# Kernel tuning notes

Hardware: AMD Instinct MI355X
Metric: run time of the kernel (lower is better)

Reference implementation:

```python
import jax, jax.numpy as jnp
import numpy as np

D = 512  # d_model
B, H, W = 32, 32, 32


def _conv1x1(x, w, b):
    # x: [B,C,H,W], w: [O,C], b: [O] -> [B,O,H,W]
    return jnp.einsum('oc,bchw->bohw', w, x) + b[None, :, None, None]


def setup_inputs() -> dict:
    key = jax.random.key(0)
    ks = jax.random.split(key, 16)
    std = 0.01  # init.normal_(m.weight, 0, 0.01)
    inp = {
        'out0': jax.random.normal(ks[0], (B, D, H, W), jnp.float32),
        'out1': jax.random.normal(ks[1], (B, D, H, W), jnp.float32),
        'out2': jax.random.normal(ks[2], (B, D, H, W), jnp.float32),
        'gamma': jax.random.uniform(ks[3], (1,), jnp.float32),
        'gamma_1': jax.random.uniform(ks[4], (1,), jnp.float32),
        'gamma_2': jax.random.uniform(ks[5], (1,), jnp.float32),
        'W_in1': std * jax.random.normal(ks[6], (D, D), jnp.float32),
        'b_in1': jnp.zeros((D,), jnp.float32),
        'W_in2': std * jax.random.normal(ks[7], (D, D), jnp.float32),
        'b_in2': jnp.zeros((D,), jnp.float32),
        'W_in3': std * jax.random.normal(ks[8], (D, D), jnp.float32),
        'b_in3': jnp.zeros((D,), jnp.float32),
        'W_trans': std * jax.random.normal(ks[9], (3 * D, 3 * D), jnp.float32),
        'b_trans': jnp.zeros((3 * D,), jnp.float32),
        'W_out1': std * jax.random.normal(ks[10], (D, D), jnp.float32),
        'b_out1': jnp.zeros((D,), jnp.float32),
        'W_out2': std * jax.random.normal(ks[11], (D, D), jnp.float32),
        'b_out2': jnp.zeros((D,), jnp.float32),
        'W_out3': std * jax.random.normal(ks[12], (D, D), jnp.float32),
        'b_out3': jnp.zeros((D,), jnp.float32),
    }
    return inp


def reference(out0, out1, out2, gamma, gamma_1, gamma_2,
              W_in1, b_in1, W_in2, b_in2, W_in3, b_in3,
              W_trans, b_trans, W_out1, b_out1, W_out2, b_out2,
              W_out3, b_out3):
    out_sim = gamma[0] * out0
    out_sim_1 = gamma_1[0] * out1
    out_sim_2 = gamma_2[0] * out2
    H_1 = _conv1x1(out_sim, W_in1, b_in1)
    H_2 = _conv1x1(out_sim_1, W_in2, b_in2)
    H_3 = _conv1x1(out_sim_2, W_in3, b_in3)
    H_cat = jnp.concatenate((H_1, H_2, H_3), axis=1)  # [B,3D,H,W]
    H_tra = _conv1x1(H_cat, W_trans, b_trans)
    s0, s1, s2 = H_tra[:, :D], H_tra[:, D:2 * D], H_tra[:, 2 * D:]
    H_4 = jax.nn.sigmoid(_conv1x1(s0, W_out1, b_out1))
    H_5 = jax.nn.sigmoid(_conv1x1(s1, W_out2, b_out2))
    H_6 = jax.nn.sigmoid(_conv1x1(s2, W_out3, b_out3))
    H_st = jnp.stack((H_4, H_5, H_6), axis=0)  # [3,B,D,H,W]
    H_all = jax.nn.softmax(H_st, axis=0)
    fused = H_all[0] * out_sim + H_all[1] * out_sim_1 + H_all[2] * out_sim_2
    return fused
```

## Files before the change

### kernel.cpp

```cpp
#include <hip/hip_runtime.h>
#include <hip/hip_bf16.h>

#define NPIX 32768
#define DCH 512
#define HWSZ 1024
#define WSQ (DCH * DCH)
#define WTR (3 * DCH * 3 * DCH)

typedef __bf16 bf16x8_t __attribute__((ext_vector_type(8)));
typedef float f32x4_t __attribute__((ext_vector_type(4)));
typedef float f32x16_t __attribute__((ext_vector_type(16)));
typedef int i32x4_t __attribute__((ext_vector_type(4)));
typedef int i32x8_t __attribute__((ext_vector_type(8)));
typedef unsigned short u16x8_t __attribute__((ext_vector_type(8)));
typedef unsigned short u16x4_t __attribute__((ext_vector_type(4)));

static __device__ __forceinline__ unsigned short f2bf(float f) {
    return __builtin_bit_cast(unsigned short, __float2bfloat16(f));
}
static __device__ __forceinline__ float bf2f(unsigned short u) {
    unsigned v = (unsigned)u << 16;
    return __builtin_bit_cast(float, v);
}

__global__ __launch_bounds__(256)
void cvt_all(const float* __restrict__ w0, const float* __restrict__ w1,
             const float* __restrict__ w2, const float* __restrict__ w3,
             const float* __restrict__ w4, const float* __restrict__ w5,
             const float* __restrict__ w6,
             __hip_bfloat16* __restrict__ d, unsigned char* __restrict__ d8,
             const float* __restrict__ b0, const float* __restrict__ b1,
             const float* __restrict__ b2, const float* __restrict__ b3,
             const float* __restrict__ b4, const float* __restrict__ b5,
             float* __restrict__ biasd)
{
    const int NB = (6 * WSQ + WTR) >> 10;
    const int bid = blockIdx.x;
    if (bid == 2 * NB) {
        for (int idx = threadIdx.x; idx < 3072; idx += 256) {
            const int r = idx >> 9, off = idx & 511;
            const float* s = (r == 0) ? b0 : (r == 1) ? b1 : (r == 2) ? b2
                           : (r == 3) ? b3 : (r == 4) ? b4 : b5;
            biasd[idx] = s[off];
        }
        return;
    }
    const bool do8 = (bid >= NB);
    const int i = ((do8 ? bid - NB : bid) * 256 + threadIdx.x) * 4;
    const float* src;
    int off;
    if (i < 3 * WSQ) {
        int r = i >> 18;
        src = (r == 0) ? w0 : ((r == 1) ? w1 : w2);
        off = i - r * WSQ;
    } else if (i < 3 * WSQ + WTR) {
        src = w3; off = i - 3 * WSQ;
    } else {
        int j = i - 3 * WSQ - WTR;
        int r = j >> 18;
        src = (r == 0) ? w4 : ((r == 1) ? w5 : w6);
        off = j - r * WSQ;
    }
    float4 f = *(const float4*)(src + off);
    if (do8) {
        int dw = __builtin_amdgcn_cvt_pk_fp8_f32(f.x, f.y, 0, false);
        dw     = __builtin_amdgcn_cvt_pk_fp8_f32(f.z, f.w, dw, true);
        *(int*)(d8 + i) = dw;
    } else {
        u16x4_t v;
        v[0] = f2bf(f.x); v[1] = f2bf(f.y); v[2] = f2bf(f.z); v[3] = f2bf(f.w);
        *(u16x4_t*)((unsigned short*)d + i) = v;
    }
}

__global__ __launch_bounds__(256)
void stage_transpose(const float* __restrict__ x0, const float* __restrict__ x1,
                     const float* __restrict__ x2,
                     const float* __restrict__ gp0, const float* __restrict__ gp1,
                     const float* __restrict__ gp2,
                     __hip_bfloat16* __restrict__ XbT,
                     unsigned char* __restrict__ Xb8, int emit8)
{
    __shared__ float tile[64][65];
    const int hw0 = blockIdx.x * 64;
    const int c0  = blockIdx.y * 64;
    const int bz  = blockIdx.z;
    const int br  = bz >> 5;
    const int b   = bz & 31;
    const float* x = (br == 0) ? x0 : ((br == 1) ? x1 : x2);
    const float g  = ((br == 0) ? gp0 : ((br == 1) ? gp1 : gp2))[0];
    const int t = threadIdx.x;

    const int qh = (t & 15) * 4;
    const int rb = t >> 4;
    const float* src = x + (size_t)b * (DCH * HWSZ) + (size_t)c0 * HWSZ + hw0;
#pragma unroll
    for (int i = 0; i < 4; ++i) {
        const int ci = rb + i * 16;
        float4 v = *(const float4*)(src + (size_t)ci * HWSZ + qh);
        v.x *= g; v.y *= g; v.z *= g; v.w *= g;
        *(float4*)&tile[ci][qh] = v;
    }
    __syncthreads();

    const int hwr = t >> 2;
    const int cch = (t & 3) * 16;
    const size_t nrow = (size_t)br * NPIX + b * HWSZ + hw0 + hwr;
    float vals[16];
#pragma unroll
    for (int e = 0; e < 16; ++e) vals[e] = tile[cch + e][hwr];

    __hip_bfloat16* dst = XbT + nrow * DCH + c0 + cch;
    u16x8_t v0, v1;
#pragma unroll
    for (int e = 0; e < 8; ++e) v0[e] = f2bf(vals[e]);
#pragma unroll
    for (int e = 0; e < 8; ++e) v1[e] = f2bf(vals[8 + e]);
    *(u16x8_t*)dst = v0;
    *((u16x8_t*)dst + 1) = v1;

    if (emit8) {
        i32x4_t w;
#pragma unroll
        for (int q = 0; q < 4; ++q) {
            int dw = __builtin_amdgcn_cvt_pk_fp8_f32(vals[4 * q], vals[4 * q + 1], 0, false);
            dw     = __builtin_amdgcn_cvt_pk_fp8_f32(vals[4 * q + 2], vals[4 * q + 3], dw, true);
            w[q] = dw;
        }
        *(i32x4_t*)(Xb8 + nrow * DCH + c0 + cch) = w;
    }
}

struct pair4 { i32x4_t lo, hi; };

__global__ __launch_bounds__(256, 2)
void gemm_f8(const unsigned char* __restrict__ A, int lda,
             const unsigned char* __restrict__ B, int ldb,
             const float* __restrict__ bias,
             void* __restrict__ Cv, int ldc, int coff0,
             int K, int NO, int TPB, int brA, int brB,
             int bstride, int cstride, int cmode)
{
    __shared__ __align__(16) unsigned char smem[73728];
    const int tid  = threadIdx.x;
    const int lane = tid & 63;
    const int wave = tid >> 6;
    const int wm = wave >> 1, wn = wave & 1;
    const int l31 = lane & 31;
    const int h   = lane >> 5;

    const int per  = gridDim.x >> 3;
    const int flat = (blockIdx.x & 7) * per + (blockIdx.x >> 3);
    const int br   = flat / TPB;
    const int rem  = flat - br * TPB;
    const int nt = rem / NO, ot = rem % NO;
    const int n0 = nt * 256, o0 = ot * 128;
    const int NT = K >> 6;

    A    += (size_t)br * (size_t)brA;
    B    += (size_t)br * (size_t)brB;
    bias += br * bstride;
    const int coff = coff0 + br * cstride;

    auto stage = [&](int t, unsigned bufb) {
#pragma unroll
        for (int p = 0; p < 6; ++p) {
            const int f = tid + p * 256;
            if (p < 4) {
                const int row = f >> 2, cidx = f & 3;
                const int gch = ((cidx ^ (row & 3) ^ ((row >> 2) & 3)) << 4);
                const unsigned char* ga = A + (size_t)(n0 + row) * lda + t * 64 + gch;
                __builtin_amdgcn_global_load_lds(
                    (const __attribute__((address_space(1))) unsigned int*)ga,
                    (__attribute__((address_space(3))) unsigned int*)(smem + bufb + f * 16),
                    16, 0, 0);
            } else {
                const int fb = f - 1024;
                const int row = fb >> 2, cidx = fb & 3;
                const int gch = ((cidx ^ (row & 3) ^ ((row >> 2) & 3)) << 4);
                const unsigned char* gb = B + (size_t)(o0 + row) * ldb + t * 64 + gch;
                __builtin_amdgcn_global_load_lds(
                    (const __attribute__((address_space(1))) unsigned int*)gb,
                    (__attribute__((address_space(3))) unsigned int*)(smem + bufb + 16384u + fb * 16),
                    16, 0, 0);
            }
        }
    };

#define DSR(dst, a) asm volatile("ds_read_b128 %0, %1" : "=v"(dst) : "v"(a))

    f32x16_t acc[4][2];
#pragma unroll
    for (int mf = 0; mf < 4; ++mf)
#pragma unroll
        for (int nf = 0; nf < 2; ++nf)
#pragma unroll
            for (int e = 0; e < 16; ++e) acc[mf][nf][e] = 0.f;

    unsigned addrA[4], addrB[2];
#pragma unroll
    for (int mf = 0; mf < 4; ++mf) {
        const int r = wm * 128 + mf * 32 + l31;
        const int s = (r & 3) ^ ((r >> 2) & 3);
        addrA[mf] = (unsigned)(r << 6) + (unsigned)((((h << 1)) ^ s) << 4);
    }
#pragma unroll
    for (int nf = 0; nf < 2; ++nf) {
        const int rb = wn * 64 + nf * 32 + l31;
        const int s = (rb & 3) ^ ((rb >> 2) & 3);
        addrB[nf] = 16384u + (unsigned)(rb << 6) + (unsigned)((((h << 1)) ^ s) << 4);
    }

    stage(0, 0u); stage(1, 24576u);
    asm volatile("s_waitcnt vmcnt(6)");
    __builtin_amdgcn_s_barrier();

    unsigned cur = 0u, nxt = 24576u, thr = 49152u;
    for (int t = 0; t < NT; ++t) {
        if (t + 2 < NT) stage(t + 2, thr);

        pair4 a_[4], b_[2];
#pragma unroll
        for (int mf = 0; mf < 4; ++mf) {
            DSR(a_[mf].lo, cur + addrA[mf]);
            DSR(a_[mf].hi, (cur + addrA[mf]) ^ 16u);
        }
#pragma unroll
        for (int nf = 0; nf < 2; ++nf) {
            DSR(b_[nf].lo, cur + addrB[nf]);
            DSR(b_[nf].hi, (cur + addrB[nf]) ^ 16u);
        }
        asm volatile("s_waitcnt lgkmcnt(0)");
        __builtin_amdgcn_sched_barrier(0);

        __builtin_amdgcn_s_setprio(1);
#pragma unroll
        for (int mf = 0; mf < 4; ++mf)
#pragma unroll
            for (int nf = 0; nf < 2; ++nf)
                acc[mf][nf] = __builtin_amdgcn_mfma_scale_f32_32x32x64_f8f6f4(
                    __builtin_bit_cast(i32x8_t, a_[mf]),
                    __builtin_bit_cast(i32x8_t, b_[nf]), acc[mf][nf],
                    0, 0, 0, 0x7F7F7F7F, 0, 0x7F7F7F7F);
        __builtin_amdgcn_s_setprio(0);

        if (t + 2 < NT)      { asm volatile("s_waitcnt vmcnt(6)"); }
        else if (t + 1 < NT) { asm volatile("s_waitcnt vmcnt(0)"); }
        __builtin_amdgcn_s_barrier();
        const unsigned tmp = cur; cur = nxt; nxt = thr; thr = tmp;
    }
#undef DSR

    if (cmode == 0) {
        __hip_bfloat16* C = (__hip_bfloat16*)Cv;
#pragma unroll
        for (int nf = 0; nf < 2; ++nf) {
            const int col = o0 + wn * 64 + nf * 32 + l31;
            const float bv = bias[col];
#pragma unroll
            for (int mf = 0; mf < 4; ++mf)
#pragma unroll
                for (int rg = 0; rg < 16; ++rg) {
                    const int row = n0 + wm * 128 + mf * 32 + (rg & 3) + ((rg >> 2) << 3) + (h << 2);
                    C[(size_t)row * ldc + coff + col] = __float2bfloat16(acc[mf][nf][rg] + bv);
                }
        }
    } else {
        unsigned char* C8 = (unsigned char*)Cv;
#pragma unroll
        for (int nf = 0; nf < 2; ++nf) {
            const int col = o0 + wn * 64 + nf * 32 + l31;
            const float bv = bias[col];
#pragma unroll
            for (int mf = 0; mf < 4; ++mf)
#pragma unroll
                for (int q = 0; q < 4; ++q) {
                    int dw = __builtin_amdgcn_cvt_pk_fp8_f32(acc[mf][nf][4 * q] + bv,
                                                             acc[mf][nf][4 * q + 1] + bv, 0, false);
                    dw     = __builtin_amdgcn_cvt_pk_fp8_f32(acc[mf][nf][4 * q + 2] + bv,
                                                             acc[mf][nf][4 * q + 3] + bv, dw, true);
                    const int row = n0 + wm * 128 + mf * 32 + 8 * q + (h << 2);
                    const size_t base = (size_t)row * ldc + coff + col;
                    const unsigned u = (unsigned)dw;
                    C8[base]           = (unsigned char)u;
                    C8[base + ldc]     = (unsigned char)(u >> 8);
                    C8[base + 2 * ldc] = (unsigned char)(u >> 16);
                    C8[base + 3 * ldc] = (unsigned char)(u >> 24);
                }
        }
    }
}

__global__ __launch_bounds__(512, 2)
void gemm256(const __hip_bfloat16* __restrict__ A, int lda,
             const __hip_bfloat16* __restrict__ B, int ldb,
             const float* __restrict__ bias,
             __hip_bfloat16* __restrict__ C, int ldc, int coff0,
             int K, int NO, int TPB, int brA, int brB, int bstride,
             int cstride, int trans_out)
{
    __shared__ __align__(16) unsigned char smem[131072];
    const int tid  = threadIdx.x;
    const int lane = tid & 63;
    const int wave = tid >> 6;
    const int wm   = wave >> 2;
    const int wn   = wave & 3;
    const int l16  = lane & 15;
    const int l4   = lane >> 4;

    const int per  = gridDim.x >> 3;
    const int flat = (blockIdx.x & 7) * per + (blockIdx.x >> 3);
    const int br   = flat / TPB;
    const int rem  = flat - br * TPB;
    const int nt   = rem / NO;
    const int ot   = rem - nt * NO;
    const int n0 = nt * 256;
    const int o0 = ot * 256;
    const int NT = K >> 6;

    A    += (size_t)br * (size_t)brA;
    B    += (size_t)br * (size_t)brB;
    bias += br * bstride;
    const int coff = coff0 + br * cstride;

    const unsigned xorv = (unsigned)((l16 & 7) << 4);
    unsigned baseA[2], baseB[2];
#pragma unroll
    for (int kk = 0; kk < 2; ++kk) {
        const unsigned ko = ((unsigned)(kk * 64 + l4 * 16)) ^ xorv;
        baseA[kk] = (unsigned)((wm * 128 + l16) * 128) + ko;
        baseB[kk] = 32768u + (unsigned)((wn * 64 + l16) * 128) + ko;
    }

    const int rr  = lane >> 3;
    const int kel = 8 * ((lane & 7) ^ rr);

    auto stageA = [&](int t, int half) {
        const unsigned dst = (unsigned)((t & 1) * 65536 + half * 16384 + wave * 2048);
        const __hip_bfloat16* g = A + (size_t)(n0 + half * 128 + wave * 16 + rr) * lda + t * 64 + kel;
#pragma unroll
        for (int s = 0; s < 2; ++s) {
            __builtin_amdgcn_global_load_lds(
                (const __attribute__((address_space(1))) unsigned int*)(g + (size_t)s * 8 * lda),
                (__attribute__((address_space(3))) unsigned int*)(smem + dst + s * 1024),
                16, 0, 0);
        }
    };
    auto stageB = [&](int t, int half) {
        const unsigned dst = (unsigned)((t & 1) * 65536 + 32768 + half * 16384 + wave * 2048);
        const __hip_bfloat16* g = B + (size_t)(o0 + half * 128 + wave * 16 + rr) * ldb + t * 64 + kel;
#pragma unroll
        for (int s = 0; s < 2; ++s) {
            __builtin_amdgcn_global_load_lds(
                (const __attribute__((address_space(1))) unsigned int*)(g + (size_t)s * 8 * ldb),
                (__attribute__((address_space(3))) unsigned int*)(smem + dst + s * 1024),
                16, 0, 0);
        }
    };

#define DSRO(dst, addr, OFF) \
    asm volatile("ds_read_b128 %0, %1 offset:" #OFF : "=v"(dst) : "v"(addr))
#define BC(x) __builtin_bit_cast(bf16x8_t, x)

    stageA(0, 0); stageA(0, 1); stageB(0, 0); stageB(0, 1);
    stageA(1, 0); stageA(1, 1); stageB(1, 0); stageB(1, 1);
    asm volatile("s_waitcnt vmcnt(8)");
    __builtin_amdgcn_s_barrier();

    f32x4_t aR[4][2], a2[4][2], bA[2][2], bB[2][2];
    f32x4_t acc[8][4];
#pragma unroll
    for (int m = 0; m < 8; ++m)
#pragma unroll
        for (int n = 0; n < 4; ++n) acc[m][n] = (f32x4_t){0.f, 0.f, 0.f, 0.f};

    {
        unsigned a0 = baseA[0], a1 = baseA[1], b0 = baseB[0], b1 = baseB[1];
        DSRO(aR[0][0], a0, 0);    DSRO(aR[1][0], a0, 2048);
        DSRO(aR[2][0], a0, 4096); DSRO(aR[3][0], a0, 6144);
        DSRO(aR[0][1], a1, 0);    DSRO(aR[1][1], a1, 2048);
        DSRO(aR[2][1], a1, 4096); DSRO(aR[3][1], a1, 6144);
        DSRO(bA[0][0], b0, 0);    DSRO(bA[1][0], b0, 2048);
        DSRO(bA[0][1], b1, 0);    DSRO(bA[1][1], b1, 2048);
    }

    unsigned cb = 0;
    for (int t = 0; t < NT; ++t) {
        const unsigned cbn = cb ^ 65536u;
        const unsigned a0 = cb + baseA[0], a1 = cb + baseA[1];
        const unsigned b0 = cb + baseB[0], b1 = cb + baseB[1];

        asm volatile("s_waitcnt lgkmcnt(0)");
        __builtin_amdgcn_sched_barrier(0);
        DSRO(bB[0][0], b0, 4096); DSRO(bB[1][0], b0, 6144);
        DSRO(bB[0][1], b1, 4096); DSRO(bB[1][1], b1, 6144);
        __builtin_amdgcn_sched_barrier(0);
        __builtin_amdgcn_s_setprio(1);
#pragma unroll
        for (int m = 0; m < 4; ++m)
#pragma unroll
            for (int n = 0; n < 2; ++n)
#pragma unroll
                for (int kk = 0; kk < 2; ++kk)
                    acc[m][n] = __builtin_amdgcn_mfma_f32_16x16x32_bf16(BC(aR[m][kk]), BC(bA[n][kk]), acc[m][n], 0, 0, 0);
        __builtin_amdgcn_s_setprio(0);
        __builtin_amdgcn_s_barrier();

        asm volatile("s_waitcnt lgkmcnt(0)");
        __builtin_amdgcn_sched_barrier(0);
        DSRO(a2[0][0], a0, 8192);  DSRO(a2[1][0], a0, 10240);
        DSRO(a2[2][0], a0, 12288); DSRO(a2[3][0], a0, 14336);
        DSRO(a2[0][1], a1, 8192);  DSRO(a2[1][1], a1, 10240);
        DSRO(a2[2][1], a1, 12288); DSRO(a2[3][1], a1, 14336);
        __builtin_amdgcn_sched_barrier(0);
        __builtin_amdgcn_s_setprio(1);
#pragma unroll
        for (int m = 0; m < 4; ++m)
#pragma unroll
            for (int n = 0; n < 2; ++n)
#pragma unroll
                for (int kk = 0; kk < 2; ++kk)
                    acc[m][n + 2] = __builtin_amdgcn_mfma_f32_16x16x32_bf16(BC(aR[m][kk]), BC(bB[n][kk]), acc[m][n + 2], 0, 0, 0);
        __builtin_amdgcn_s_setprio(0);
        __builtin_amdgcn_s_barrier();

        asm volatile("s_waitcnt lgkmcnt(0)");
        __builtin_amdgcn_sched_barrier(0);
        if (t + 2 < NT) { stageB(t + 2, 0); stageB(t + 2, 1); }
        __builtin_amdgcn_sched_barrier(0);
        __builtin_amdgcn_s_setprio(1);
#pragma unroll
        for (int m = 0; m < 4; ++m)
#pragma unroll
            for (int n = 0; n < 2; ++n)
#pragma unroll
                for (int kk = 0; kk < 2; ++kk)
                    acc[m + 4][n] = __builtin_amdgcn_mfma_f32_16x16x32_bf16(BC(a2[m][kk]), BC(bA[n][kk]), acc[m + 4][n], 0, 0, 0);
        __builtin_amdgcn_s_setprio(0);
        if (t + 2 < NT)        { asm volatile("s_waitcnt vmcnt(4)"); }
        else if (t + 2 == NT)  { asm volatile("s_waitcnt vmcnt(0)"); }
        __builtin_amdgcn_s_barrier();

        if (t + 1 < NT) {
            const unsigned na0 = cbn + baseA[0], na1 = cbn + baseA[1];
            const unsigned nb0 = cbn + baseB[0], nb1 = cbn + baseB[1];
            DSRO(aR[0][0], na0, 0);    DSRO(aR[1][0], na0, 2048);
            DSRO(aR[2][0], na0, 4096); DSRO(aR[3][0], na0, 6144);
            DSRO(aR[0][1], na1, 0);    DSRO(aR[1][1], na1, 2048);
            DSRO(aR[2][1], na1, 4096); DSRO(aR[3][1], na1, 6144);
            DSRO(bA[0][0], nb0, 0);    DSRO(bA[1][0], nb0, 2048);
            DSRO(bA[0][1], nb1, 0);    DSRO(bA[1][1], nb1, 2048);
        }
        if (t + 2 < NT) { stageA(t + 2, 0); stageA(t + 2, 1); }
        __builtin_amdgcn_sched_barrier(0);
        __builtin_amdgcn_s_setprio(1);
#pragma unroll
        for (int m = 0; m < 4; ++m)
#pragma unroll
            for (int n = 0; n < 2; ++n)
#pragma unroll
                for (int kk = 0; kk < 2; ++kk)
                    acc[m + 4][n + 2] = __builtin_amdgcn_mfma_f32_16x16x32_bf16(BC(a2[m][kk]), BC(bB[n][kk]), acc[m + 4][n + 2], 0, 0, 0);
        __builtin_amdgcn_s_setprio(0);
        cb = cbn;
    }

    if (!trans_out) {
#pragma unroll
        for (int n = 0; n < 4; ++n) {
            const int oc = o0 + wn * 64 + n * 16 + l16;
            const float bv = bias[oc];
#pragma unroll
            for (int m = 0; m < 8; ++m)
#pragma unroll
                for (int r = 0; r < 4; ++r) {
                    const int nr = n0 + wm * 128 + m * 16 + l4 * 4 + r;
                    C[(size_t)nr * ldc + coff + oc] = __float2bfloat16(acc[m][n][r] + bv);
                }
        }
    } else {
        __syncthreads();
#pragma unroll
        for (int n = 0; n < 4; ++n) {
            const int ocl = wn * 64 + n * 16 + l16;
            const float bv = bias[o0 + ocl];
#pragma unroll
            for (int m = 0; m < 8; ++m)
#pragma unroll
                for (int r = 0; r < 4; ++r) {
                    const int nrow = wm * 128 + m * 16 + l4 * 4 + r;
                    const unsigned phys = (unsigned)nrow * 512u
                        + (((unsigned)ocl * 2u) ^ (((unsigned)(nrow & 7)) << 4));
                    *(unsigned short*)(smem + phys) = f2bf(acc[m][n][r] + bv);
                }
        }
        __syncthreads();
        const int ol = tid >> 1;
        const int nh = (tid & 1) * 128;
        __hip_bfloat16* dst = C + (size_t)(coff + o0 + ol) * ldc + n0 + nh;
#pragma unroll
        for (int j8 = 0; j8 < 16; ++j8) {
            u16x8_t v;
#pragma unroll
            for (int e = 0; e < 8; ++e) {
                const int n2 = nh + j8 * 8 + e;
                v[e] = *(const unsigned short*)(smem + (unsigned)n2 * 512u
                        + ((((unsigned)ol * 2u) ^ ((unsigned)e << 4))));
            }
            *(u16x8_t*)((unsigned short*)dst + j8 * 8) = v;
        }
    }
#undef DSRO
#undef BC
}

__global__ __launch_bounds__(256)
void final_v2(const __hip_bfloat16* __restrict__ G,
              const __hip_bfloat16* __restrict__ Xb,
              float* __restrict__ out)
{
    __shared__ float tile[64][68];
    const int n0  = blockIdx.x * 64;
    const int b   = n0 >> 10;
    const int hw0 = n0 & (HWSZ - 1);
    const int t   = threadIdx.x;
    const int nl  = t >> 2;
    const int cg  = (t & 3) * 16;
    const int n   = n0 + nl;
    const unsigned short* gr = (const unsigned short*)G + (size_t)n * 1536;
    const unsigned short* xr = (const unsigned short*)Xb + (size_t)n * 512;
    const int seg = t & 3;
    float* outb = out + (size_t)b * (DCH * HWSZ) + hw0;

    for (int c0 = 0; c0 < DCH; c0 += 64) {
        u16x8_t gl[3][2], xl[3][2];
#pragma unroll
        for (int i = 0; i < 3; ++i) {
            gl[i][0] = *(const u16x8_t*)(gr + i * 512 + c0 + cg);
            gl[i][1] = *(const u16x8_t*)(gr + i * 512 + c0 + cg + 8);
            xl[i][0] = *(const u16x8_t*)(xr + (size_t)i * NPIX * 512 + c0 + cg);
            xl[i][1] = *(const u16x8_t*)(xr + (size_t)i * NPIX * 512 + c0 + cg + 8);
        }
#pragma unroll
        for (int e = 0; e < 16; ++e) {
            const int hh = e >> 3, w = e & 7;
            const float s0 = bf2f(gl[0][hh][w]);
            const float s1 = bf2f(gl[1][hh][w]);
            const float s2 = bf2f(gl[2][hh][w]);
            const float g0 = 1.0f / (1.0f + __expf(-s0));
            const float g1 = 1.0f / (1.0f + __expf(-s1));
            const float g2 = 1.0f / (1.0f + __expf(-s2));
            const float e0 = __expf(g0), e1 = __expf(g1), e2 = __expf(g2);
            const float inv = 1.0f / (e0 + e1 + e2);
            tile[cg + e][nl] = inv * (e0 * bf2f(xl[0][hh][w])
                                    + e1 * bf2f(xl[1][hh][w])
                                    + e2 * bf2f(xl[2][hh][w]));
        }
        __syncthreads();
#pragma unroll
        for (int j4 = 0; j4 < 4; ++j4) {
            float4 v = *(const float4*)&tile[nl][seg * 16 + j4 * 4];
            *(float4*)(outb + (size_t)(c0 + nl) * HWSZ + seg * 16 + j4 * 4) = v;
        }
        __syncthreads();
    }
}

__global__ __launch_bounds__(256)
void final_fuse(const __hip_bfloat16* __restrict__ G,
                const float* __restrict__ x0, const float* __restrict__ x1,
                const float* __restrict__ x2,
                const float* __restrict__ gp0, const float* __restrict__ gp1,
                const float* __restrict__ gp2,
                float* __restrict__ out)
{
    const int n  = blockIdx.x * 256 + threadIdx.x;
    const int b  = n >> 10;
    const int hw = n & (HWSZ - 1);
    const int c0 = blockIdx.y * 64;
    const float ga0 = gp0[0], ga1 = gp1[0], ga2 = gp2[0];
    for (int cc = 0; cc < 64; ++cc) {
        const int c = c0 + cc;
        const float s0 = __bfloat162float(G[(size_t)c * NPIX + n]);
        const float s1 = __bfloat162float(G[(size_t)(c + DCH) * NPIX + n]);
        const float s2 = __bfloat162float(G[(size_t)(c + 2 * DCH) * NPIX + n]);
        const float g0v = 1.0f / (1.0f + __expf(-s0));
        const float g1v = 1.0f / (1.0f + __expf(-s1));
        const float g2v = 1.0f / (1.0f + __expf(-s2));
        const float e0 = __expf(g0v), e1 = __expf(g1v), e2 = __expf(g2v);
        const float inv = 1.0f / (e0 + e1 + e2);
        const size_t xo = (size_t)b * (DCH * HWSZ) + (size_t)c * HWSZ + hw;
        out[xo] = inv * (e0 * ga0 * x0[xo] + e1 * ga1 * x1[xo] + e2 * ga2 * x2[xo]);
    }
}

extern "C" void kernel_launch(void* const* d_in, const int* in_sizes, int n_in,
                              void* d_out, int out_size, void* d_ws, size_t ws_size,
                              hipStream_t stream)
{
    const float* out0   = (const float*)d_in[0];
    const float* out1   = (const float*)d_in[1];
    const float* out2   = (const float*)d_in[2];
    const float* gamma0 = (const float*)d_in[3];
    const float* gamma1 = (const float*)d_in[4];
    const float* gamma2 = (const float*)d_in[5];
    const float* W_in1  = (const float*)d_in[6];
    const float* W_in2  = (const float*)d_in[8];
    const float* W_in3  = (const float*)d_in[10];
    const float* b_in1  = (const float*)d_in[7];
    const float* b_in2  = (const float*)d_in[9];
    const float* b_in3  = (const float*)d_in[11];
    const float* W_tr   = (const float*)d_in[12];
    const float* b_tr   = (const float*)d_in[13];
    const float* W_o1   = (const float*)d_in[14];
    const float* b_o1   = (const float*)d_in[15];
    const float* W_o2   = (const float*)d_in[16];
    const float* b_o2   = (const float*)d_in[17];
    const float* W_o3   = (const float*)d_in[18];
    const float* b_o3   = (const float*)d_in[19];
    float* outp = (float*)d_out;

    unsigned char* ws = (unsigned char*)d_ws;
    const size_t SZ_ACT  = (size_t)3 * NPIX * DCH * 2;
    const size_t SZ_ACT8 = (size_t)3 * NPIX * DCH;
    const size_t WB_BF16 = (size_t)(6 * WSQ + WTR) * 2;
    const size_t WB_FP8  = (size_t)(6 * WSQ + WTR);
    const size_t NEED    = 2 * SZ_ACT + SZ_ACT8 + WB_BF16 + WB_FP8 + 16384;
    const bool   big     = (ws_size >= NEED);

    __hip_bfloat16* buf0 = (__hip_bfloat16*)ws;
    unsigned char*  P8   = ws + SZ_ACT;
    unsigned char*  Q    = ws + SZ_ACT + SZ_ACT8;
    unsigned char*  wtop = big ? (ws + 2 * SZ_ACT + SZ_ACT8) : (ws + 2 * SZ_ACT);
    __hip_bfloat16* Wb     = (__hip_bfloat16*)wtop;
    __hip_bfloat16* Wb_tr  = Wb + 3 * WSQ;
    __hip_bfloat16* Wb_o   = Wb_tr + WTR;
    unsigned char*  Wf8    = wtop + WB_BF16;
    unsigned char*  Win8   = Wf8;
    unsigned char*  Wtr8   = Wf8 + 3 * WSQ;
    unsigned char*  Wo8    = Wf8 + 3 * WSQ + WTR;
    float*          biasWS = (float*)(wtop + WB_BF16 + WB_FP8);

    const int NB = (6 * WSQ + WTR) >> 10;
    cvt_all<<<2 * NB + 1, 256, 0, stream>>>(
        W_in1, W_in2, W_in3, W_tr, W_o1, W_o2, W_o3, Wb, Wf8,
        b_in1, b_in2, b_in3, b_o1, b_o2, b_o3, biasWS);

    stage_transpose<<<dim3(16, 8, 96), 256, 0, stream>>>(
        out0, out1, out2, gamma0, gamma1, gamma2, buf0, P8, big ? 1 : 0);

    if (big) {
        gemm_f8<<<dim3(1536), 256, 0, stream>>>(
            P8, DCH, Win8, DCH, biasWS, Q, 3 * DCH, 0,
            DCH, 4, 512, NPIX * DCH, WSQ, DCH, DCH, 1);
        gemm_f8<<<dim3(1536), 256, 0, stream>>>(
            Q, 3 * DCH, Wtr8, 3 * DCH, b_tr, P8, 3 * DCH, 0,
            3 * DCH, 12, 1536, 0, 0, 0, 0, 1);
        gemm_f8<<<dim3(1536), 256, 0, stream>>>(
            P8, 3 * DCH, Wo8, DCH, biasWS + 3 * DCH, Q, 3 * DCH, 0,
            DCH, 4, 512, DCH, WSQ, DCH, DCH, 0);
        final_v2<<<dim3(NPIX / 64), 256, 0, stream>>>((const __hip_bfloat16*)Q, buf0, outp);
    } else {
        __hip_bfloat16* buf1 = (__hip_bfloat16*)(ws + SZ_ACT);
        gemm256<<<dim3(768), 512, 0, stream>>>(
            buf0, DCH, Wb, DCH, biasWS,
            buf1, 3 * DCH, 0, DCH, 2, 256, NPIX * DCH, WSQ, DCH, DCH, 0);
        gemm256<<<dim3(768), 512, 0, stream>>>(
            buf1, 3 * DCH, Wb_tr, 3 * DCH, b_tr,
            buf0, 3 * DCH, 0, 3 * DCH, 6, 768, 0, 0, 0, 0, 0);
        gemm256<<<dim3(768), 512, 0, stream>>>(
            buf0, 3 * DCH, Wb_o, DCH, biasWS + 3 * DCH,
            buf1, NPIX, 0, DCH, 2, 256, DCH, WSQ, DCH, DCH, 1);
        final_fuse<<<dim3(NPIX / 256, DCH / 64), 256, 0, stream>>>(
            buf1, out0, out1, out2, gamma0, gamma1, gamma2, outp);
    }
}
```

Before: 317.8 us.

## Drop bf16 activation copy in fp8 path; transpose gate output and reuse final_fuse

In the fp8 path, stage_transpose no longer writes the bf16 transposed copy of the scaled inputs. The final fp8 GEMM now writes its gate output transposed (channel-major) through an LDS-staged, swizzled epilogue, so the existing final_fuse kernel can read the original fp32 inputs directly. This removes a large bf16 write and a later read, and makes the final stage use exact fp32 inputs. The cost is an extra LDS round trip with barriers in the GEMM epilogue, and final_fuse rereads the fp32 inputs.

New measurement: 321.0 us. No clear change (+1.0%).

```diff
diff --git a/kernel.cpp b/kernel.cpp
--- a/kernel.cpp
+++ b/kernel.cpp
@@ -79,7 +79,7 @@
                      const float* __restrict__ gp0, const float* __restrict__ gp1,
                      const float* __restrict__ gp2,
                      __hip_bfloat16* __restrict__ XbT,
-                     unsigned char* __restrict__ Xb8, int emit8)
+                     unsigned char* __restrict__ Xb8, int emitbf, int emit8)
 {
     __shared__ float tile[64][65];
     const int hw0 = blockIdx.x * 64;
@@ -110,15 +110,16 @@
 #pragma unroll
     for (int e = 0; e < 16; ++e) vals[e] = tile[cch + e][hwr];
 
-    __hip_bfloat16* dst = XbT + nrow * DCH + c0 + cch;
-    u16x8_t v0, v1;
-#pragma unroll
-    for (int e = 0; e < 8; ++e) v0[e] = f2bf(vals[e]);
-#pragma unroll
-    for (int e = 0; e < 8; ++e) v1[e] = f2bf(vals[8 + e]);
-    *(u16x8_t*)dst = v0;
-    *((u16x8_t*)dst + 1) = v1;
-
+    if (emitbf) {
+        __hip_bfloat16* dst = XbT + nrow * DCH + c0 + cch;
+        u16x8_t v0, v1;
+#pragma unroll
+        for (int e = 0; e < 8; ++e) v0[e] = f2bf(vals[e]);
+#pragma unroll
+        for (int e = 0; e < 8; ++e) v1[e] = f2bf(vals[8 + e]);
+        *(u16x8_t*)dst = v0;
+        *((u16x8_t*)dst + 1) = v1;
+    }
     if (emit8) {
         i32x4_t w;
 #pragma unroll
@@ -265,7 +266,7 @@
                     C[(size_t)row * ldc + coff + col] = __float2bfloat16(acc[mf][nf][rg] + bv);
                 }
         }
-    } else {
+    } else if (cmode == 1) {
         unsigned char* C8 = (unsigned char*)Cv;
 #pragma unroll
         for (int nf = 0; nf < 2; ++nf) {
@@ -287,6 +288,34 @@
                     C8[base + 2 * ldc] = (unsigned char)(u >> 16);
                     C8[base + 3 * ldc] = (unsigned char)(u >> 24);
                 }
+        }
+    } else {
+        __hip_bfloat16* C = (__hip_bfloat16*)Cv;
+        __syncthreads();
+#pragma unroll
+        for (int nf = 0; nf < 2; ++nf) {
+            const int cl = wn * 64 + nf * 32 + l31;
+            const float bv = bias[o0 + cl];
+            const unsigned sw = ((unsigned)(cl & 7)) << 4;
+#pragma unroll
+            for (int mf = 0; mf < 4; ++mf)
+#pragma unroll
+                for (int rg = 0; rg < 16; ++rg) {
+                    const int r = wm * 128 + mf * 32 + (rg & 3) + ((rg >> 2) << 3) + (h << 2);
+                    *(unsigned short*)(smem + (unsigned)cl * 512u + (((unsigned)r * 2u) ^ sw)) =
+                        f2bf(acc[mf][nf][rg] + bv);
+                }
+        }
+        __syncthreads();
+        const int cl   = tid >> 1;
+        const int half = tid & 1;
+        const unsigned sw = ((unsigned)(cl & 7)) << 4;
+        __hip_bfloat16* dst = C + (size_t)(coff + o0 + cl) * (size_t)ldc + n0 + half * 128;
+#pragma unroll
+        for (int j8 = 0; j8 < 16; ++j8) {
+            const unsigned byteL = (unsigned)cl * 512u
+                + ((((unsigned)(half * 128 + j8 * 8)) * 2u) ^ sw);
+            *(u16x8_t*)((unsigned short*)dst + j8 * 8) = *(const u16x8_t*)(smem + byteL);
         }
     }
 }
@@ -512,58 +541,6 @@
     }
 #undef DSRO
 #undef BC
-}
-
-__global__ __launch_bounds__(256)
-void final_v2(const __hip_bfloat16* __restrict__ G,
-              const __hip_bfloat16* __restrict__ Xb,
-              float* __restrict__ out)
-{
-    __shared__ float tile[64][68];
-    const int n0  = blockIdx.x * 64;
-    const int b   = n0 >> 10;
-    const int hw0 = n0 & (HWSZ - 1);
-    const int t   = threadIdx.x;
-    const int nl  = t >> 2;
-    const int cg  = (t & 3) * 16;
-    const int n   = n0 + nl;
-    const unsigned short* gr = (const unsigned short*)G + (size_t)n * 1536;
-    const unsigned short* xr = (const unsigned short*)Xb + (size_t)n * 512;
-    const int seg = t & 3;
-    float* outb = out + (size_t)b * (DCH * HWSZ) + hw0;
-
-    for (int c0 = 0; c0 < DCH; c0 += 64) {
-        u16x8_t gl[3][2], xl[3][2];
-#pragma unroll
-        for (int i = 0; i < 3; ++i) {
-            gl[i][0] = *(const u16x8_t*)(gr + i * 512 + c0 + cg);
-            gl[i][1] = *(const u16x8_t*)(gr + i * 512 + c0 + cg + 8);
-            xl[i][0] = *(const u16x8_t*)(xr + (size_t)i * NPIX * 512 + c0 + cg);
-            xl[i][1] = *(const u16x8_t*)(xr + (size_t)i * NPIX * 512 + c0 + cg + 8);
-        }
-#pragma unroll
-        for (int e = 0; e < 16; ++e) {
-            const int hh = e >> 3, w = e & 7;
-            const float s0 = bf2f(gl[0][hh][w]);
-            const float s1 = bf2f(gl[1][hh][w]);
-            const float s2 = bf2f(gl[2][hh][w]);
-            const float g0 = 1.0f / (1.0f + __expf(-s0));
-            const float g1 = 1.0f / (1.0f + __expf(-s1));
-            const float g2 = 1.0f / (1.0f + __expf(-s2));
-            const float e0 = __expf(g0), e1 = __expf(g1), e2 = __expf(g2);
-            const float inv = 1.0f / (e0 + e1 + e2);
-            tile[cg + e][nl] = inv * (e0 * bf2f(xl[0][hh][w])
-                                    + e1 * bf2f(xl[1][hh][w])
-                                    + e2 * bf2f(xl[2][hh][w]));
-        }
-        __syncthreads();
-#pragma unroll
-        for (int j4 = 0; j4 < 4; ++j4) {
-            float4 v = *(const float4*)&tile[nl][seg * 16 + j4 * 4];
-            *(float4*)(outb + (size_t)(c0 + nl) * HWSZ + seg * 16 + j4 * 4) = v;
-        }
-        __syncthreads();
-    }
 }
 
 __global__ __launch_bounds__(256)
@@ -647,7 +624,8 @@
         b_in1, b_in2, b_in3, b_o1, b_o2, b_o3, biasWS);
 
     stage_transpose<<<dim3(16, 8, 96), 256, 0, stream>>>(
-        out0, out1, out2, gamma0, gamma1, gamma2, buf0, P8, big ? 1 : 0);
+        out0, out1, out2, gamma0, gamma1, gamma2,
+        buf0, P8, big ? 0 : 1, big ? 1 : 0);
 
     if (big) {
         gemm_f8<<<dim3(1536), 256, 0, stream>>>(
@@ -657,9 +635,10 @@
             Q, 3 * DCH, Wtr8, 3 * DCH, b_tr, P8, 3 * DCH, 0,
             3 * DCH, 12, 1536, 0, 0, 0, 0, 1);
         gemm_f8<<<dim3(1536), 256, 0, stream>>>(
-            P8, 3 * DCH, Wo8, DCH, biasWS + 3 * DCH, Q, 3 * DCH, 0,
-            DCH, 4, 512, DCH, WSQ, DCH, DCH, 0);
-        final_v2<<<dim3(NPIX / 64), 256, 0, stream>>>((const __hip_bfloat16*)Q, buf0, outp);
+            P8, 3 * DCH, Wo8, DCH, biasWS + 3 * DCH, buf0, NPIX, 0,
+            DCH, 4, 512, DCH, WSQ, DCH, DCH, 2);
+        final_fuse<<<dim3(NPIX / 256, DCH / 64), 256, 0, stream>>>(
+            buf0, out0, out1, out2, gamma0, gamma1, gamma2, outp);
     } else {
         __hip_bfloat16* buf1 = (__hip_bfloat16*)(ws + SZ_ACT);
         gemm256<<<dim3(768), 512, 0, stream>>>(
```
